# Optimization experiments

Measured on AMD Instinct MI355X. Metric: run time of the kernel, lower is better.

Reference implementation:

```python
import jax, jax.numpy as jnp
import numpy as np

B, CI, GEN, CON, CO, FAC = 32768, 128, 512, 256, 64, 128
CLIP = 5.0
# h_0 layout: [gen_state, con_state, co_mean, co_std, gen_input, factor]
SPLITS = [GEN, GEN + CON, GEN + CON + CO, GEN + CON + 2 * CO, GEN + CON + 3 * CO]


def _gru(x, h, Wih, bih, Whh, bhh, H):
    # x_all = x @ Wih.T + bih ; chunks z, r, n
    xa = x @ Wih.T + bih
    xz, xr, xn = jnp.split(xa, 3, axis=1)
    ha = h @ Whh[: 2 * H].T + bhh[: 2 * H]
    hz, hr = jnp.split(ha, 2, axis=1)
    z = jax.nn.sigmoid(xz + hz)
    r = jax.nn.sigmoid(xr + hr)
    # note: torch code computes (r * hidden) @ W_n.T (left-assoc * and @)
    hn = (r * h) @ Whh[2 * H :].T + bhh[2 * H :]
    n = jnp.tanh(xn + hn)
    h_new = z * h + (1.0 - z) * n
    return jnp.clip(h_new, -CLIP, CLIP)


def setup_inputs() -> dict:
    key = jax.random.key(0)
    ks = jax.random.split(key, 12)
    rn = lambda k, shape, scale: (jax.random.normal(k, shape, jnp.float32) * scale)
    return {
        "input": rn(ks[0], (B, 2 * CI), 1.0),
        "h_0": rn(ks[1], (B, GEN + CON + 3 * CO + FAC), 1.0),
        "eps": rn(ks[2], (B, CO), 1.0),
        "gen_Wih": rn(ks[3], (3 * GEN, CO), 1.0 / np.sqrt(CO)),
        "gen_bih": jnp.concatenate([jnp.ones(2 * GEN, jnp.float32), jnp.zeros(GEN, jnp.float32)]),
        "gen_Whh": rn(ks[4], (3 * GEN, GEN), 1.0 / np.sqrt(GEN)),
        "gen_bhh": jnp.zeros(3 * GEN, jnp.float32),
        "con_Wih": rn(ks[5], (3 * CON, 2 * CI + FAC), 1.0 / np.sqrt(2 * CI + FAC)),
        "con_bih": jnp.concatenate([jnp.ones(2 * CON, jnp.float32), jnp.zeros(CON, jnp.float32)]),
        "con_Whh": rn(ks[6], (3 * CON, CON), 1.0 / np.sqrt(CON)),
        "con_bhh": jnp.zeros(3 * CON, jnp.float32),
        "fac_W": rn(ks[7], (FAC, GEN), 1.0 / np.sqrt(GEN)),
        "co_W": rn(ks[8], (2 * CO, CON), 1.0 / np.sqrt(CON)),
        "co_b": jnp.zeros(2 * CO, jnp.float32),
    }


def reference(input, h_0, eps, gen_Wih, gen_bih, gen_Whh, gen_bhh,
              con_Wih, con_bih, con_Whh, con_bhh, fac_W, co_W, co_b):
    gen_state, con_state, co_mean, co_std, gen_input, factor = jnp.split(h_0, SPLITS, axis=1)
    # controller path (use_con=True): dropout is identity (rate=0 / eval)
    con_input = jnp.concatenate([input, factor], axis=1)
    con_state = _gru(con_input, con_state, con_Wih, con_bih, con_Whh, con_bhh, CON)
    co_params = con_state @ co_W.T + co_b
    co_mean, co_logvar = jnp.split(co_params, 2, axis=1)
    co_std = jnp.exp(0.5 * co_logvar)  # sqrt(exp(logvar))
    gen_input = co_mean + co_std * eps  # rsample (sample_posteriors=True)
    gen_state = _gru(gen_input, gen_state, gen_Wih, gen_bih, gen_Whh, gen_bhh, GEN)
    # kernel-normalized linear: L2-normalize each output row over in_features
    norm = jnp.sqrt(jnp.sum(fac_W * fac_W, axis=1, keepdims=True))
    normed_W = fac_W / jnp.maximum(norm, 1e-12)
    factor = gen_state @ normed_W.T
    return jnp.concatenate([gen_state, con_state, co_mean, co_std, gen_input, factor], axis=1)
```

## Files before the change

### kernel.cpp

```cpp
#include <hip/hip_runtime.h>


typedef short  s16x8 __attribute__((ext_vector_type(8)));
typedef float  f32x4 __attribute__((ext_vector_type(4)));
typedef unsigned short ush;

#define OUTP 1088
#define NROW 32768

__device__ __forceinline__ int swz(int k, int row) {
  return (k & ~63) | ((k & 63) ^ ((row & 7) << 3));
}
__device__ __forceinline__ ush f2bf(float f) {
  union { float f; unsigned int u; } v; v.f = f;
  unsigned int u = v.u;
  return (ush)((u + 0x7FFFu + ((u >> 16) & 1u)) >> 16);
}
__device__ __forceinline__ float bf2f(ush b) {
  union { unsigned int u; float f; } v; v.u = ((unsigned int)b) << 16;
  return v.f;
}
__device__ __forceinline__ float sigm(float x) { return 1.f / (1.f + __expf(-x)); }
__device__ __forceinline__ float tanh_(float x) { return 2.f / (1.f + __expf(-2.f * x)) - 1.f; }

__device__ __forceinline__ f32x4 mfma16(s16x8 a, s16x8 b, f32x4 c) {
  return __builtin_amdgcn_mfma_f32_16x16x32_bf16(a, b, c, 0, 0, 0);
}
__device__ __forceinline__ s16x8 ldb8(const ush* p) {
  return *reinterpret_cast<const s16x8*>(p);
}
__device__ __forceinline__ void gld16(const ush* g, ush* l) {
  __builtin_amdgcn_global_load_lds(
      (const __attribute__((address_space(1))) unsigned int*)g,
      (__attribute__((address_space(3))) unsigned int*)l, 16, 0, 0);
}
__device__ __forceinline__ ushort4 pack4(float4 a) {
  ushort4 o; o.x = f2bf(a.x); o.y = f2bf(a.y); o.z = f2bf(a.z); o.w = f2bf(a.w);
  return o;
}

__global__ void prepA_kernel(const float* __restrict__ in, const float* __restrict__ h0,
                             ush* __restrict__ Acon, ush* __restrict__ Agen) {
  int t = blockIdx.x * 256 + threadIdx.x;
  int row = t / 144, c = t % 144;
  if (c < 80) {
    int c8 = c * 8;
    const float* src;
    if (c8 < 256)      src = &in[(size_t)row * 256 + c8];
    else if (c8 < 384) src = &h0[(size_t)row * OUTP + 960 + (c8 - 256)];
    else               src = &h0[(size_t)row * OUTP + 512 + (c8 - 384)];
    float4 a = *reinterpret_cast<const float4*>(src);
    float4 b = *reinterpret_cast<const float4*>(src + 4);
    ushort4* d = reinterpret_cast<ushort4*>(&Acon[(size_t)row * 640 + swz(c8, row)]);
    d[0] = pack4(a); d[1] = pack4(b);
  } else {
    int c8 = (c - 80) * 8;
    float4 a = *reinterpret_cast<const float4*>(&h0[(size_t)row * OUTP + c8]);
    float4 b = *reinterpret_cast<const float4*>(&h0[(size_t)row * OUTP + c8 + 4]);
    ushort4* d = reinterpret_cast<ushort4*>(&Agen[(size_t)row * 576 + swz(64 + c8, row)]);
    d[0] = pack4(a); d[1] = pack4(b);
  }
}

__global__ void packBcon_kernel(const float* __restrict__ wih, const float* __restrict__ whh,
                                ush* __restrict__ B1, ush* __restrict__ B2) {
  int r = blockIdx.x;
  int c4 = threadIdx.x * 4;
  float4 v = (c4 < 384) ? *reinterpret_cast<const float4*>(&wih[(size_t)r * 384 + c4])
                        : *reinterpret_cast<const float4*>(&whh[(size_t)r * 256 + (c4 - 384)]);
  int pc = swz(c4, r);
  ush* dst = (r < 512) ? &B1[(size_t)r * 640 + pc] : &B2[(size_t)(r - 512) * 640 + pc];
  *reinterpret_cast<ushort4*>(dst) = pack4(v);
}

__global__ void packBgen_kernel(const float* __restrict__ wih, const float* __restrict__ whh,
                                ush* __restrict__ B1, ush* __restrict__ B2) {
  int r = blockIdx.x;
  int c4 = threadIdx.x * 4;
  float4 v = (c4 < 64) ? *reinterpret_cast<const float4*>(&wih[(size_t)r * 64 + c4])
                       : *reinterpret_cast<const float4*>(&whh[(size_t)r * 512 + (c4 - 64)]);
  int pc = swz(c4, r);
  ush* dst = (r < 1024) ? &B1[(size_t)r * 576 + pc] : &B2[(size_t)(r - 1024) * 576 + pc];
  *reinterpret_cast<ushort4*>(dst) = pack4(v);
}

__global__ void cvtco_kernel(const float* __restrict__ src, ush* __restrict__ dst) {
  int i = blockIdx.x * 256 + threadIdx.x;
  int row = i >> 6, c4 = (i & 63) * 4;
  float4 v = *reinterpret_cast<const float4*>(&src[(size_t)row * 256 + c4]);
  *reinterpret_cast<ushort4*>(&dst[(size_t)row * 256 + swz(c4, row)]) = pack4(v);
}

__global__ void facnorm_kernel(const float* __restrict__ w, ush* __restrict__ dst) {
  int row = blockIdx.x;
  int lane = threadIdx.x;
  float v[8]; float s = 0.f;
  #pragma unroll
  for (int i = 0; i < 8; ++i) { v[i] = w[row * 512 + lane * 8 + i]; s += v[i] * v[i]; }
  #pragma unroll
  for (int off = 32; off; off >>= 1) s += __shfl_xor(s, off);
  float scale = 1.f / fmaxf(sqrtf(s), 1e-12f);
  int pc = swz(lane * 8, row);
  #pragma unroll
  for (int i = 0; i < 8; ++i) dst[row * 512 + pc + i] = f2bf(v[i] * scale);
}

__global__ void rsample_kernel(const float* __restrict__ eps, float* __restrict__ out,
                               ush* __restrict__ Agen) {
  int t = blockIdx.x * 256 + threadIdx.x;
  int m = t >> 6, j = t & 63;
  float mean = out[(size_t)m * OUTP + 768 + j];
  float sd   = out[(size_t)m * OUTP + 832 + j];
  float g = mean + sd * eps[(size_t)m * 64 + j];
  out[(size_t)m * OUTP + 896 + j] = g;
  Agen[(size_t)m * 576 + (j ^ ((m & 7) << 3))] = f2bf(g);
}

template<int EPI, int KTOT, int KA1, int SA1, int SA2, int SB,
         int NT, int NHALF, int SAH, int OOFS, int SHN>
__global__ __launch_bounds__(512, 2) void gemmD_kernel(
    const ush* __restrict__ A1, const ush* __restrict__ A2,
    const ush* __restrict__ B,
    const float* __restrict__ bih, const float* __restrict__ bhh,
    const ush* __restrict__ Ah,
    const ush* __restrict__ zbuf,
    ush* __restrict__ st1, ush* __restrict__ st2,
    float* __restrict__ out)
{
  __shared__ __align__(16) ush S[2 * 2 * 128 * 64];
  const int nwg = gridDim.x;
  const int wg = (blockIdx.x & 7) * (nwg >> 3) + (blockIdx.x >> 3);
  const int mt = wg / NT, nt = wg % NT;
  const int m0 = mt * 128, n0 = nt * 128;
  const int tid = threadIdx.x;
  const int wv = tid >> 6, lane = tid & 63;
  const int ln = lane & 15, lk = lane >> 4;
  const int wm = wv >> 2, wn = wv & 3;
  const int srow = lane >> 3;
  const int scol = (lane & 7) * 8;
  const int xs = (ln & 7) << 3;
  constexpr int NK = KTOT / 64;

  f32x4 acc[4][2] = {};

  const int ar0 = wv * 16 + srow, ar1 = wv * 16 + 8 + srow;
  const ush* a1p0 = A1 + (size_t)(m0 + ar0) * SA1 + scol;
  const ush* a1p1 = A1 + (size_t)(m0 + ar1) * SA1 + scol;
  const ush* a2p0 = A2 + (size_t)(m0 + ar0) * SA2 + scol;
  const ush* a2p1 = A2 + (size_t)(m0 + ar1) * SA2 + scol;
  const ush* bp0  = B  + (size_t)(n0 + ar0) * SB  + scol;
  const ush* bp1  = B  + (size_t)(n0 + ar1) * SB  + scol;
  ush* ldsA0 = &S[(wv * 16) * 64];
  ush* ldsA1 = &S[(wv * 16 + 8) * 64];

  auto STAGE = [&](int t, int b) {
    const int k0 = t * 64;
    ush* As = ldsA0 + b * 16384;
    ush* As1 = ldsA1 + b * 16384;
    if (KA1 >= KTOT || k0 < KA1) {
      gld16(a1p0 + k0, As);
      gld16(a1p1 + k0, As1);
    } else {
      gld16(a2p0 + (k0 - KA1), As);
      gld16(a2p1 + (k0 - KA1), As1);
    }
    gld16(bp0 + k0, As + 8192);
    gld16(bp1 + k0, As1 + 8192);
  };

  STAGE(0, 0);
  #pragma unroll
  for (int t = 0; t < NK; ++t) {
    if (t + 1 < NK) {
      STAGE(t + 1, (t + 1) & 1);
      asm volatile("s_waitcnt vmcnt(4)" ::: "memory");
    } else {
      asm volatile("s_waitcnt vmcnt(0)" ::: "memory");
    }
    __builtin_amdgcn_s_barrier();
    const ush* As = &S[(t & 1) * 16384];
    const ush* Bs = As + 8192;
    __builtin_amdgcn_s_setprio(1);
    #pragma unroll
    for (int kk2 = 0; kk2 < 2; ++kk2) {
      const int kb = (kk2 * 32 + lk * 8) ^ xs;
      s16x8 af[4], bf[2];
      #pragma unroll
      for (int i = 0; i < 4; ++i) af[i] = ldb8(&As[(wm * 64 + i * 16 + ln) * 64 + kb]);
      #pragma unroll
      for (int j = 0; j < 2; ++j) bf[j] = ldb8(&Bs[(wn * 32 + j * 16 + ln) * 64 + kb]);
      #pragma unroll
      for (int i = 0; i < 4; ++i)
        #pragma unroll
        for (int j = 0; j < 2; ++j)
          acc[i][j] = mfma16(af[i], bf[j], acc[i][j]);
    }
    __builtin_amdgcn_s_setprio(0);
    asm volatile("s_waitcnt lgkmcnt(0)" ::: "memory");
    __builtin_amdgcn_s_barrier();
  }

  ush* Ls = S;

  if constexpr (EPI == 0) {
    const bool isz = (n0 < NHALF);
    #pragma unroll
    for (int i = 0; i < 4; ++i) {
      #pragma unroll
      for (int j = 0; j < 2; ++j) {
        const int jl = wn * 32 + j * 16 + ln;
        const int jg = n0 + jl;
        const float bb = bih[jg] + bhh[jg];
        #pragma unroll
        for (int r = 0; r < 4; ++r) {
          const int rl = wm * 64 + i * 16 + lk * 4 + r;
          float sv = sigm(acc[i][j][r] + bb);
          if (!isz) sv *= bf2f(Ah[(size_t)(m0 + rl) * SAH + swz(jg - NHALF, rl)]);
          Ls[rl * 128 + (jl ^ ((rl & 7) << 3))] = f2bf(sv);
        }
      }
    }
    __syncthreads();
    #pragma unroll
    for (int q = 0; q < 4; ++q) {
      int idx = q * 512 + tid;
      int r = idx >> 4, c8 = (idx & 15) * 8;
      float4 v = *reinterpret_cast<const float4*>(&Ls[r * 128 + (c8 ^ ((r & 7) << 3))]);
      if (isz) *reinterpret_cast<float4*>(&st1[(size_t)(m0 + r) * NHALF + n0 + c8]) = v;
      else     *reinterpret_cast<float4*>(&st2[(size_t)(m0 + r) * NHALF +
                                               swz(n0 - NHALF + c8, r)]) = v;
    }
  } else {
    #pragma unroll
    for (int i = 0; i < 4; ++i) {
      #pragma unroll
      for (int j = 0; j < 2; ++j) {
        const int jl = wn * 32 + j * 16 + ln;
        const int jg = n0 + jl;
        const float bb = bih[2 * NHALF + jg] + bhh[2 * NHALF + jg];
        #pragma unroll
        for (int r = 0; r < 4; ++r) {
          const int rl = wm * 64 + i * 16 + lk * 4 + r;
          const size_t m = (size_t)(m0 + rl);
          float n = tanh_(acc[i][j][r] + bb);
          float z = bf2f(zbuf[m * NHALF + jg]);
          float h = bf2f(Ah[m * SAH + swz(jg, rl)]);
          float hv = fminf(fmaxf(z * h + (1.f - z) * n, -5.f), 5.f);
          Ls[rl * 128 + (jl ^ ((rl & 7) << 3))] = f2bf(hv);
        }
      }
    }
    __syncthreads();
    #pragma unroll
    for (int q = 0; q < 4; ++q) {
      int idx = q * 512 + tid;
      int r = idx >> 4, c8 = (idx & 15) * 8;
      union { float4 f; ush u[8]; } U;
      U.f = *reinterpret_cast<const float4*>(&Ls[r * 128 + (c8 ^ ((r & 7) << 3))]);
      *reinterpret_cast<float4*>(&st1[(size_t)(m0 + r) * SHN + swz(n0 + c8, r)]) = U.f;
      float4 o0 = { bf2f(U.u[0]), bf2f(U.u[1]), bf2f(U.u[2]), bf2f(U.u[3]) };
      float4 o1 = { bf2f(U.u[4]), bf2f(U.u[5]), bf2f(U.u[6]), bf2f(U.u[7]) };
      float* ob = &out[(size_t)(m0 + r) * OUTP + OOFS + n0 + c8];
      *reinterpret_cast<float4*>(ob) = o0;
      *reinterpret_cast<float4*>(ob + 4) = o1;
    }
  }
}

template<int EPI, int KTOT, int KA1, int SA1, int SA2, int SB,
         int NT, int NHALF, int SAH, int OOFS, int SHN>
__global__ __launch_bounds__(256, 4) void gemm_kernel(
    const ush* __restrict__ A1, const ush* __restrict__ A2,
    const ush* __restrict__ B,
    const float* __restrict__ bih, const float* __restrict__ bhh,
    const ush* __restrict__ Ah,
    const ush* __restrict__ zbuf,
    ush* __restrict__ st1, ush* __restrict__ st2,
    float* __restrict__ out)
{
  __shared__ ush S[2 * 128 * 64];
  const int nwg = gridDim.x;
  const int wg = (blockIdx.x & 7) * (nwg >> 3) + (blockIdx.x >> 3);
  const int mt = wg / NT, nt = wg % NT;
  const int m0 = mt * 128, n0 = nt * 128;
  const int tid = threadIdx.x;
  const int w = tid >> 6, lane = tid & 63;
  const int ln = lane & 15, lk = lane >> 4;
  const int wm = w >> 1, wn = w & 1;
  const int srow = lane >> 3;
  const int scol = (lane & 7) * 8;
  constexpr int NK = KTOT / 64;
  const int xs = (ln & 7) << 3;

  f32x4 acc[4][4] = {};
  ush* As = S;
  ush* Bs = S + 8192;

  #pragma unroll
  for (int ks = 0; ks < NK; ++ks) {
    const int k0 = ks * 64;
    const ush* Ab; size_t sa; int kk;
    if (KA1 >= KTOT || k0 < KA1) { Ab = A1; sa = SA1; kk = k0; }
    else                         { Ab = A2; sa = SA2; kk = k0 - KA1; }
    #pragma unroll
    for (int p = 0; p < 4; ++p) {
      int r0 = p * 32 + w * 8;
      gld16(Ab + (size_t)(m0 + r0 + srow) * sa + kk + scol, &As[r0 * 64]);
    }
    #pragma unroll
    for (int p = 0; p < 4; ++p) {
      int r0 = p * 32 + w * 8;
      gld16(B + (size_t)(n0 + r0 + srow) * SB + k0 + scol, &Bs[r0 * 64]);
    }
    asm volatile("s_waitcnt vmcnt(0)" ::: "memory");
    __syncthreads();
    #pragma unroll
    for (int kk2 = 0; kk2 < 2; ++kk2) {
      const int kb = (kk2 * 32 + lk * 8) ^ xs;
      s16x8 af[4], bf[4];
      #pragma unroll
      for (int i = 0; i < 4; ++i) af[i] = ldb8(&As[(wm * 64 + i * 16 + ln) * 64 + kb]);
      #pragma unroll
      for (int i = 0; i < 4; ++i) bf[i] = ldb8(&Bs[(wn * 64 + i * 16 + ln) * 64 + kb]);
      #pragma unroll
      for (int i = 0; i < 4; ++i)
        #pragma unroll
        for (int j = 0; j < 4; ++j)
          acc[i][j] = mfma16(af[i], bf[j], acc[i][j]);
    }
    __syncthreads();
  }

  if constexpr (EPI == 2) {
    #pragma unroll
    for (int i = 0; i < 4; ++i) {
      #pragma unroll
      for (int j = 0; j < 4; ++j) {
        const int jg = n0 + wn * 64 + j * 16 + ln;
        const float bb = bih[jg];
        #pragma unroll
        for (int r = 0; r < 4; ++r) {
          const size_t m = (size_t)(m0 + wm * 64 + i * 16 + lk * 4 + r);
          float v = acc[i][j][r] + bb;
          if (jg < 64) out[m * OUTP + 768 + jg] = v;
          else         out[m * OUTP + 832 + (jg - 64)] = __expf(0.5f * v);
        }
      }
    }
  } else {
    #pragma unroll
    for (int i = 0; i < 4; ++i)
      #pragma unroll
      for (int j = 0; j < 4; ++j) {
        const int jg = n0 + wn * 64 + j * 16 + ln;
        #pragma unroll
        for (int r = 0; r < 4; ++r)
          out[(size_t)(m0 + wm * 64 + i * 16 + lk * 4 + r) * OUTP + 960 + jg] =
              acc[i][j][r];
      }
  }
}

extern "C" void kernel_launch(void* const* d_in, const int* in_sizes, int n_in,
                              void* d_out, int out_size, void* d_ws, size_t ws_size,
                              hipStream_t stream) {
  const float* input   = (const float*)d_in[0];
  const float* h0      = (const float*)d_in[1];
  const float* eps     = (const float*)d_in[2];
  const float* gen_Wih = (const float*)d_in[3];
  const float* gen_bih = (const float*)d_in[4];
  const float* gen_Whh = (const float*)d_in[5];
  const float* gen_bhh = (const float*)d_in[6];
  const float* con_Wih = (const float*)d_in[7];
  const float* con_bih = (const float*)d_in[8];
  const float* con_Whh = (const float*)d_in[9];
  const float* con_bhh = (const float*)d_in[10];
  const float* fac_W   = (const float*)d_in[11];
  const float* co_W    = (const float*)d_in[12];
  const float* co_b    = (const float*)d_in[13];
  float* out = (float*)d_out;

  ush* ws = (ush*)d_ws;
  ush* A_gen  = ws;
  ush* A_con  = A_gen + (size_t)NROW * 576;
  ush* z_con  = A_con + (size_t)NROW * 640;
  ush* rh_con = z_con + (size_t)NROW * 256;
  ush* B1c    = rh_con + (size_t)NROW * 256;
  ush* B2c    = B1c + 512 * 640;
  ush* B1g    = B2c + 256 * 640;
  ush* B2g    = B1g + 1024 * 576;
  ush* coWb   = B2g + 512 * 576;
  ush* facWn  = coWb + 128 * 256;
  ush* z_gen  = A_con;
  ush* rh_gen = z_con;

  packBcon_kernel<<<768, 160, 0, stream>>>(con_Wih, con_Whh, B1c, B2c);
  packBgen_kernel<<<1536, 144, 0, stream>>>(gen_Wih, gen_Whh, B1g, B2g);
  cvtco_kernel<<<32, 256, 0, stream>>>(co_W, coWb);
  facnorm_kernel<<<128, 64, 0, stream>>>(fac_W, facWn);
  prepA_kernel<<<18432, 256, 0, stream>>>(input, h0, A_con, A_gen);

  gemmD_kernel<0, 640, 640, 640, 640, 640, 4, 256, 640, 0, 0>
      <<<1024, 512, 0, stream>>>(A_con, A_con, B1c, con_bih, con_bhh,
                                 A_con + 384, nullptr, z_con, rh_con, out);
  gemmD_kernel<1, 640, 384, 640, 256, 640, 2, 256, 640, 512, 640>
      <<<512, 512, 0, stream>>>(A_con, rh_con, B2c, con_bih, con_bhh,
                                A_con + 384, z_con, A_con + 384, nullptr, out);
  gemm_kernel<2, 256, 256, 640, 640, 256, 1, 64, 640, 0, 0>
      <<<256, 256, 0, stream>>>(A_con + 384, A_con + 384, coWb, co_b, co_b,
                                nullptr, nullptr, nullptr, nullptr, out);
  rsample_kernel<<<8192, 256, 0, stream>>>(eps, out, A_gen);

  gemmD_kernel<0, 576, 576, 576, 576, 576, 8, 512, 576, 0, 0>
      <<<2048, 512, 0, stream>>>(A_gen, A_gen, B1g, gen_bih, gen_bhh,
                                 A_gen + 64, nullptr, z_gen, rh_gen, out);
  gemmD_kernel<1, 576, 64, 576, 512, 576, 4, 512, 576, 0, 576>
      <<<1024, 512, 0, stream>>>(A_gen, rh_gen, B2g, gen_bih, gen_bhh,
                                 A_gen + 64, z_gen, A_gen + 64, nullptr, out);
  gemm_kernel<3, 512, 512, 576, 576, 512, 1, 0, 576, 960, 0>
      <<<256, 256, 0, stream>>>(A_gen + 64, A_gen + 64, facWn, gen_bih, gen_bhh,
                                nullptr, nullptr, nullptr, nullptr, out);
}
```

Measured before the change: 291.5 us.

## Merge weight packing kernels, fuse rsample into co GEMM, add single-buffer gen GEMM

Three weight-conversion kernels are combined into one launch, which cuts launch overhead. The rsample step is folded into the co_W GEMM epilogue: the mean is staged through LDS and the std lane group computes the sample and writes it to both out and Agen. This removes a separate pass that re-read the output. A new single-buffered 512-thread GEMM variant with higher occupancy bounds replaces the double-buffered kernel for the first generator gate GEMM. That may change latency hiding, since it waits on global loads every K step.

Result: slower. 321.1 us (+10.2%).

```diff
diff --git a/kernel.cpp b/kernel.cpp
--- a/kernel.cpp
+++ b/kernel.cpp
@@ -62,33 +62,35 @@
   }
 }
 
-__global__ void packBcon_kernel(const float* __restrict__ wih, const float* __restrict__ whh,
-                                ush* __restrict__ B1, ush* __restrict__ B2) {
-  int r = blockIdx.x;
-  int c4 = threadIdx.x * 4;
-  float4 v = (c4 < 384) ? *reinterpret_cast<const float4*>(&wih[(size_t)r * 384 + c4])
-                        : *reinterpret_cast<const float4*>(&whh[(size_t)r * 256 + (c4 - 384)]);
-  int pc = swz(c4, r);
-  ush* dst = (r < 512) ? &B1[(size_t)r * 640 + pc] : &B2[(size_t)(r - 512) * 640 + pc];
-  *reinterpret_cast<ushort4*>(dst) = pack4(v);
-}
-
-__global__ void packBgen_kernel(const float* __restrict__ wih, const float* __restrict__ whh,
-                                ush* __restrict__ B1, ush* __restrict__ B2) {
-  int r = blockIdx.x;
-  int c4 = threadIdx.x * 4;
-  float4 v = (c4 < 64) ? *reinterpret_cast<const float4*>(&wih[(size_t)r * 64 + c4])
-                       : *reinterpret_cast<const float4*>(&whh[(size_t)r * 512 + (c4 - 64)]);
-  int pc = swz(c4, r);
-  ush* dst = (r < 1024) ? &B1[(size_t)r * 576 + pc] : &B2[(size_t)(r - 1024) * 576 + pc];
-  *reinterpret_cast<ushort4*>(dst) = pack4(v);
-}
-
-__global__ void cvtco_kernel(const float* __restrict__ src, ush* __restrict__ dst) {
-  int i = blockIdx.x * 256 + threadIdx.x;
-  int row = i >> 6, c4 = (i & 63) * 4;
-  float4 v = *reinterpret_cast<const float4*>(&src[(size_t)row * 256 + c4]);
-  *reinterpret_cast<ushort4*>(&dst[(size_t)row * 256 + swz(c4, row)]) = pack4(v);
+__global__ void prepW_kernel(const float* __restrict__ conWih, const float* __restrict__ conWhh,
+                             const float* __restrict__ genWih, const float* __restrict__ genWhh,
+                             const float* __restrict__ coW,
+                             ush* __restrict__ B1c, ush* __restrict__ B2c,
+                             ush* __restrict__ B1g, ush* __restrict__ B2g,
+                             ush* __restrict__ coWb) {
+  int b = blockIdx.x, t = threadIdx.x;
+  if (b < 480) {
+    int q = b * 256 + t;
+    int r = q / 160, c4 = (q % 160) * 4;
+    float4 v = (c4 < 384) ? *reinterpret_cast<const float4*>(&conWih[(size_t)r * 384 + c4])
+                          : *reinterpret_cast<const float4*>(&conWhh[(size_t)r * 256 + (c4 - 384)]);
+    int pc = swz(c4, r);
+    ush* dst = (r < 512) ? &B1c[(size_t)r * 640 + pc] : &B2c[(size_t)(r - 512) * 640 + pc];
+    *reinterpret_cast<ushort4*>(dst) = pack4(v);
+  } else if (b < 1344) {
+    int q = (b - 480) * 256 + t;
+    int r = q / 144, c4 = (q % 144) * 4;
+    float4 v = (c4 < 64) ? *reinterpret_cast<const float4*>(&genWih[(size_t)r * 64 + c4])
+                         : *reinterpret_cast<const float4*>(&genWhh[(size_t)r * 512 + (c4 - 64)]);
+    int pc = swz(c4, r);
+    ush* dst = (r < 1024) ? &B1g[(size_t)r * 576 + pc] : &B2g[(size_t)(r - 1024) * 576 + pc];
+    *reinterpret_cast<ushort4*>(dst) = pack4(v);
+  } else {
+    int q = (b - 1344) * 256 + t;
+    int row = q >> 6, c4 = (q & 63) * 4;
+    float4 v = *reinterpret_cast<const float4*>(&coW[(size_t)row * 256 + c4]);
+    *reinterpret_cast<ushort4*>(&coWb[(size_t)row * 256 + swz(c4, row)]) = pack4(v);
+  }
 }
 
 __global__ void facnorm_kernel(const float* __restrict__ w, ush* __restrict__ dst) {
@@ -103,17 +105,6 @@
   int pc = swz(lane * 8, row);
   #pragma unroll
   for (int i = 0; i < 8; ++i) dst[row * 512 + pc + i] = f2bf(v[i] * scale);
-}
-
-__global__ void rsample_kernel(const float* __restrict__ eps, float* __restrict__ out,
-                               ush* __restrict__ Agen) {
-  int t = blockIdx.x * 256 + threadIdx.x;
-  int m = t >> 6, j = t & 63;
-  float mean = out[(size_t)m * OUTP + 768 + j];
-  float sd   = out[(size_t)m * OUTP + 832 + j];
-  float g = mean + sd * eps[(size_t)m * 64 + j];
-  out[(size_t)m * OUTP + 896 + j] = g;
-  Agen[(size_t)m * 576 + (j ^ ((m & 7) << 3))] = f2bf(g);
 }
 
 template<int EPI, int KTOT, int KA1, int SA1, int SA2, int SB,
@@ -269,7 +260,7 @@
 
 template<int EPI, int KTOT, int KA1, int SA1, int SA2, int SB,
          int NT, int NHALF, int SAH, int OOFS, int SHN>
-__global__ __launch_bounds__(256, 4) void gemm_kernel(
+__global__ __launch_bounds__(512, 6) void gemmS_kernel(
     const ush* __restrict__ A1, const ush* __restrict__ A2,
     const ush* __restrict__ B,
     const float* __restrict__ bih, const float* __restrict__ bhh,
@@ -278,7 +269,144 @@
     ush* __restrict__ st1, ush* __restrict__ st2,
     float* __restrict__ out)
 {
-  __shared__ ush S[2 * 128 * 64];
+  __shared__ __align__(16) ush S[2 * 128 * 64];
+  const int nwg = gridDim.x;
+  const int wg = (blockIdx.x & 7) * (nwg >> 3) + (blockIdx.x >> 3);
+  const int mt = wg / NT, nt = wg % NT;
+  const int m0 = mt * 128, n0 = nt * 128;
+  const int tid = threadIdx.x;
+  const int wv = tid >> 6, lane = tid & 63;
+  const int ln = lane & 15, lk = lane >> 4;
+  const int wm = wv >> 2, wn = wv & 3;
+  const int srow = lane >> 3;
+  const int scol = (lane & 7) * 8;
+  const int xs = (ln & 7) << 3;
+  constexpr int NK = KTOT / 64;
+
+  f32x4 acc[4][2] = {};
+
+  const int ar0 = wv * 16 + srow, ar1 = wv * 16 + 8 + srow;
+  const ush* a1p0 = A1 + (size_t)(m0 + ar0) * SA1 + scol;
+  const ush* a1p1 = A1 + (size_t)(m0 + ar1) * SA1 + scol;
+  const ush* a2p0 = A2 + (size_t)(m0 + ar0) * SA2 + scol;
+  const ush* a2p1 = A2 + (size_t)(m0 + ar1) * SA2 + scol;
+  const ush* bp0  = B  + (size_t)(n0 + ar0) * SB  + scol;
+  const ush* bp1  = B  + (size_t)(n0 + ar1) * SB  + scol;
+  ush* ldsA0 = &S[(wv * 16) * 64];
+  ush* ldsA1 = &S[(wv * 16 + 8) * 64];
+
+  #pragma unroll
+  for (int t = 0; t < NK; ++t) {
+    const int k0 = t * 64;
+    if (KA1 >= KTOT || k0 < KA1) {
+      gld16(a1p0 + k0, ldsA0);
+      gld16(a1p1 + k0, ldsA1);
+    } else {
+      gld16(a2p0 + (k0 - KA1), ldsA0);
+      gld16(a2p1 + (k0 - KA1), ldsA1);
+    }
+    gld16(bp0 + k0, ldsA0 + 8192);
+    gld16(bp1 + k0, ldsA1 + 8192);
+    asm volatile("s_waitcnt vmcnt(0)" ::: "memory");
+    __syncthreads();
+    const ush* As = S;
+    const ush* Bs = S + 8192;
+    __builtin_amdgcn_s_setprio(1);
+    #pragma unroll
+    for (int kk2 = 0; kk2 < 2; ++kk2) {
+      const int kb = (kk2 * 32 + lk * 8) ^ xs;
+      s16x8 af[4], bf[2];
+      #pragma unroll
+      for (int i = 0; i < 4; ++i) af[i] = ldb8(&As[(wm * 64 + i * 16 + ln) * 64 + kb]);
+      #pragma unroll
+      for (int j = 0; j < 2; ++j) bf[j] = ldb8(&Bs[(wn * 32 + j * 16 + ln) * 64 + kb]);
+      #pragma unroll
+      for (int i = 0; i < 4; ++i)
+        #pragma unroll
+        for (int j = 0; j < 2; ++j)
+          acc[i][j] = mfma16(af[i], bf[j], acc[i][j]);
+    }
+    __builtin_amdgcn_s_setprio(0);
+    __syncthreads();
+  }
+
+  ush* Ls = S;
+
+  if constexpr (EPI == 0) {
+    const bool isz = (n0 < NHALF);
+    #pragma unroll
+    for (int i = 0; i < 4; ++i) {
+      #pragma unroll
+      for (int j = 0; j < 2; ++j) {
+        const int jl = wn * 32 + j * 16 + ln;
+        const int jg = n0 + jl;
+        const float bb = bih[jg] + bhh[jg];
+        #pragma unroll
+        for (int r = 0; r < 4; ++r) {
+          const int rl = wm * 64 + i * 16 + lk * 4 + r;
+          float sv = sigm(acc[i][j][r] + bb);
+          if (!isz) sv *= bf2f(Ah[(size_t)(m0 + rl) * SAH + swz(jg - NHALF, rl)]);
+          Ls[rl * 128 + (jl ^ ((rl & 7) << 3))] = f2bf(sv);
+        }
+      }
+    }
+    __syncthreads();
+    #pragma unroll
+    for (int q = 0; q < 4; ++q) {
+      int idx = q * 512 + tid;
+      int r = idx >> 4, c8 = (idx & 15) * 8;
+      float4 v = *reinterpret_cast<const float4*>(&Ls[r * 128 + (c8 ^ ((r & 7) << 3))]);
+      if (isz) *reinterpret_cast<float4*>(&st1[(size_t)(m0 + r) * NHALF + n0 + c8]) = v;
+      else     *reinterpret_cast<float4*>(&st2[(size_t)(m0 + r) * NHALF +
+                                               swz(n0 - NHALF + c8, r)]) = v;
+    }
+  } else {
+    #pragma unroll
+    for (int i = 0; i < 4; ++i) {
+      #pragma unroll
+      for (int j = 0; j < 2; ++j) {
+        const int jl = wn * 32 + j * 16 + ln;
+        const int jg = n0 + jl;
+        const float bb = bih[2 * NHALF + jg] + bhh[2 * NHALF + jg];
+        #pragma unroll
+        for (int r = 0; r < 4; ++r) {
+          const int rl = wm * 64 + i * 16 + lk * 4 + r;
+          const size_t m = (size_t)(m0 + rl);
+          float n = tanh_(acc[i][j][r] + bb);
+          float z = bf2f(zbuf[m * NHALF + jg]);
+          float h = bf2f(Ah[m * SAH + swz(jg, rl)]);
+          float hv = fminf(fmaxf(z * h + (1.f - z) * n, -5.f), 5.f);
+          Ls[rl * 128 + (jl ^ ((rl & 7) << 3))] = f2bf(hv);
+        }
+      }
+    }
+    __syncthreads();
+    #pragma unroll
+    for (int q = 0; q < 4; ++q) {
+      int idx = q * 512 + tid;
+      int r = idx >> 4, c8 = (idx & 15) * 8;
+      union { float4 f; ush u[8]; } U;
+      U.f = *reinterpret_cast<const float4*>(&Ls[r * 128 + (c8 ^ ((r & 7) << 3))]);
+      *reinterpret_cast<float4*>(&st1[(size_t)(m0 + r) * SHN + swz(n0 + c8, r)]) = U.f;
+      float4 o0 = { bf2f(U.u[0]), bf2f(U.u[1]), bf2f(U.u[2]), bf2f(U.u[3]) };
+      float4 o1 = { bf2f(U.u[4]), bf2f(U.u[5]), bf2f(U.u[6]), bf2f(U.u[7]) };
+      float* ob = &out[(size_t)(m0 + r) * OUTP + OOFS + n0 + c8];
+      *reinterpret_cast<float4*>(ob) = o0;
+      *reinterpret_cast<float4*>(ob + 4) = o1;
+    }
+  }
+}
+
+template<int EPI, int KTOT, int KA1, int SA1, int SA2, int SB,
+         int NT, int NHALF, int SAH, int OOFS, int SHN>
+__global__ __launch_bounds__(256, 4) void gemm_kernel(
+    const ush* __restrict__ A1, const ush* __restrict__ A2,
+    const ush* __restrict__ B,
+    const float* __restrict__ bih, const float* __restrict__ bhh,
+    const float* __restrict__ eps, ush* __restrict__ Agen,
+    float* __restrict__ out)
+{
+  __shared__ __align__(16) ush S[2 * 128 * 64];
   const int nwg = gridDim.x;
   const int wg = (blockIdx.x & 7) * (nwg >> 3) + (blockIdx.x >> 3);
   const int mt = wg / NT, nt = wg % NT;
@@ -332,18 +460,45 @@
   }
 
   if constexpr (EPI == 2) {
+    float* Lf = reinterpret_cast<float*>(S);
     #pragma unroll
     for (int i = 0; i < 4; ++i) {
       #pragma unroll
       for (int j = 0; j < 4; ++j) {
-        const int jg = n0 + wn * 64 + j * 16 + ln;
+        const int jg = wn * 64 + j * 16 + ln;
         const float bb = bih[jg];
         #pragma unroll
         for (int r = 0; r < 4; ++r) {
-          const size_t m = (size_t)(m0 + wm * 64 + i * 16 + lk * 4 + r);
+          const int rl = wm * 64 + i * 16 + lk * 4 + r;
+          const size_t m = (size_t)(m0 + rl);
           float v = acc[i][j][r] + bb;
-          if (jg < 64) out[m * OUTP + 768 + jg] = v;
-          else         out[m * OUTP + 832 + (jg - 64)] = __expf(0.5f * v);
+          if (wn == 0) {
+            out[m * OUTP + 768 + jg] = v;
+            Lf[rl * 64 + jg] = v;
+          } else {
+            out[m * OUTP + 832 + (jg - 64)] = __expf(0.5f * v);
+          }
+        }
+      }
+    }
+    __syncthreads();
+    if (wn == 1) {
+      #pragma unroll
+      for (int i = 0; i < 4; ++i) {
+        #pragma unroll
+        for (int j = 0; j < 4; ++j) {
+          const int js = j * 16 + ln;
+          const float bb = bih[64 + js];
+          #pragma unroll
+          for (int r = 0; r < 4; ++r) {
+            const int rl = wm * 64 + i * 16 + lk * 4 + r;
+            const size_t m = (size_t)(m0 + rl);
+            float sd = __expf(0.5f * (acc[i][j][r] + bb));
+            float mean = Lf[rl * 64 + js];
+            float g = mean + sd * eps[m * 64 + js];
+            out[m * OUTP + 896 + js] = g;
+            Agen[m * 576 + (js ^ ((rl & 7) << 3))] = f2bf(g);
+          }
         }
       }
     }
@@ -394,9 +549,8 @@
   ush* z_gen  = A_con;
   ush* rh_gen = z_con;
 
-  packBcon_kernel<<<768, 160, 0, stream>>>(con_Wih, con_Whh, B1c, B2c);
-  packBgen_kernel<<<1536, 144, 0, stream>>>(gen_Wih, gen_Whh, B1g, B2g);
-  cvtco_kernel<<<32, 256, 0, stream>>>(co_W, coWb);
+  prepW_kernel<<<1376, 256, 0, stream>>>(con_Wih, con_Whh, gen_Wih, gen_Whh,
+                                         co_W, B1c, B2c, B1g, B2g, coWb);
   facnorm_kernel<<<128, 64, 0, stream>>>(fac_W, facWn);
   prepA_kernel<<<18432, 256, 0, stream>>>(input, h0, A_con, A_gen);
 
@@ -408,10 +562,9 @@
                                 A_con + 384, z_con, A_con + 384, nullptr, out);
   gemm_kernel<2, 256, 256, 640, 640, 256, 1, 64, 640, 0, 0>
       <<<256, 256, 0, stream>>>(A_con + 384, A_con + 384, coWb, co_b, co_b,
-                                nullptr, nullptr, nullptr, nullptr, out);
-  rsample_kernel<<<8192, 256, 0, stream>>>(eps, out, A_gen);
-
-  gemmD_kernel<0, 576, 576, 576, 576, 576, 8, 512, 576, 0, 0>
+                                eps, A_gen, out);
+
+  gemmS_kernel<0, 576, 576, 576, 576, 576, 8, 512, 576, 0, 0>
       <<<2048, 512, 0, stream>>>(A_gen, A_gen, B1g, gen_bih, gen_bhh,
                                  A_gen + 64, nullptr, z_gen, rh_gen, out);
   gemmD_kernel<1, 576, 64, 576, 512, 576, 4, 512, 576, 0, 576>
@@ -419,5 +572,5 @@
                                  A_gen + 64, z_gen, A_gen + 64, nullptr, out);
   gemm_kernel<3, 512, 512, 576, 576, 512, 1, 0, 576, 960, 0>
       <<<256, 256, 0, stream>>>(A_gen + 64, A_gen + 64, facWn, gen_bih, gen_bhh,
-                                nullptr, nullptr, nullptr, nullptr, out);
-}
+                                nullptr, nullptr, out);
+}
```
